# Kernel optimization log

Hardware: AMD Instinct MI355X
Metric: run time of the kernel (lower is better)

## Reference

```python
import jax, jax.numpy as jnp
import numpy as np

N_NODES = 50000
N_EDGES = 600000
IN_DIM = 128
OUT_DIM = 128
NEG_SLOPE = 0.2
LN_EPS = 1e-5


def setup_inputs() -> dict:
    key = jax.random.key(0)
    ks = jax.random.split(key, 8)
    x = jax.random.normal(ks[0], (N_NODES, IN_DIM), dtype=jnp.float32)
    edge_index = jax.random.randint(ks[1], (2, N_EDGES), 0, N_NODES, dtype=jnp.int64)
    glorot = float(np.sqrt(6.0 / (IN_DIM + OUT_DIM)))
    W_l = jax.random.uniform(ks[2], (IN_DIM, OUT_DIM), jnp.float32, -glorot, glorot)
    W_r = jax.random.uniform(ks[3], (IN_DIM, OUT_DIM), jnp.float32, -glorot, glorot)
    att = jax.random.uniform(ks[4], (OUT_DIM,), jnp.float32, -glorot, glorot)
    bias = jnp.zeros((OUT_DIM,), jnp.float32)
    ln_gamma = jnp.ones((OUT_DIM,), jnp.float32)
    ln_beta = jnp.zeros((OUT_DIM,), jnp.float32)
    return {"x": x, "edge_index": edge_index, "W_l": W_l, "W_r": W_r,
            "att": att, "bias": bias, "ln_gamma": ln_gamma, "ln_beta": ln_beta}


def _gatv2_ln(x, edge_index, W_l, W_r, att, bias, ln_gamma, ln_beta):
    N = x.shape[0]
    # add self loops (PyG GATv2Conv default add_self_loops=True)
    loop = jnp.arange(N, dtype=edge_index.dtype)
    src = jnp.concatenate([edge_index[0], loop])  # [E+N]
    dst = jnp.concatenate([edge_index[1], loop])
    x_l = x @ W_l  # [N, D] transformed source features
    x_r = x @ W_r  # [N, D] transformed target features
    # GATv2 edge score: e_ij = a^T LeakyReLU(x_l[src] + x_r[dst])
    h = jax.nn.leaky_relu(x_l[src] + x_r[dst], NEG_SLOPE)  # [E+N, D]
    e = h @ att  # [E+N]
    # segment softmax over incoming edges of each dst node
    m = jax.lax.stop_gradient(jax.ops.segment_max(e, dst, num_segments=N))
    ex = jnp.exp(e - m[dst])
    denom = jax.ops.segment_sum(ex, dst, num_segments=N)
    alpha = ex / denom[dst]  # [E+N] (denom > 0 thanks to self loops)
    # weighted scatter-add aggregation (dropout=0.1 is inference no-op)
    out = jax.ops.segment_sum(alpha[:, None] * x_l[src], dst, num_segments=N)
    out = out + bias  # heads=1, concat=False -> mean over 1 head = identity
    # LayerNorm over feature dim
    mu = jnp.mean(out, axis=-1, keepdims=True)
    var = jnp.var(out, axis=-1, keepdims=True)
    return (out - mu) * jax.lax.rsqrt(var + LN_EPS) * ln_gamma + ln_beta


def reference(x, edge_index, W_l, W_r, att, bias, ln_gamma, ln_beta):
    return _gatv2_ln(x, edge_index, W_l, W_r, att, bias, ln_gamma, ln_beta)
```

## Files before the change

### kernel.cpp

```cpp
#include <hip/hip_runtime.h>
#include <hip/hip_bf16.h>


constexpr int NN  = 50000;
constexpr int NE  = 600000;
constexpr int D   = 128;
constexpr int CAP = 64;
constexpr int MT  = 80;
constexpr int GEMM_THREADS = 320;

typedef __attribute__((ext_vector_type(8))) short bf16x8;
typedef __attribute__((ext_vector_type(4))) float f32x4;

__device__ __forceinline__ ushort f2bf(float f) {
  uint u = __builtin_bit_cast(uint, f);
  return (ushort)((u + 0x7FFFu + ((u >> 16) & 1u)) >> 16);
}
__device__ __forceinline__ float2 bf2f2(uint u) {
  float2 r;
  r.x = __builtin_bit_cast(float, u << 16);
  r.y = __builtin_bit_cast(float, u & 0xFFFF0000u);
  return r;
}

__global__ __launch_bounds__(256) void k_wpack(const float* __restrict__ Wl,
    const float* __restrict__ Wr, ushort* __restrict__ wpk) {
  const int t = blockIdx.x * 256 + threadIdx.x;
  if (t >= 2 * 4 * 8 * 64) return;
  const int lane = t & 63;
  const int ct   = (t >> 6) & 7;
  const int ks   = (t >> 9) & 3;
  const int wh   = t >> 11;
  const float* W = wh ? Wr : Wl;
  const int c  = ct * 16 + (lane & 15);
  const int k0 = ks * 32 + (lane >> 4) * 8;
  ushort v[8];
#pragma unroll
  for (int j = 0; j < 8; ++j) v[j] = f2bf(W[(k0 + j) * D + c]);
  *(bf16x8*)&wpk[(size_t)t * 8] = *(bf16x8*)v;
}

__global__ __launch_bounds__(GEMM_THREADS) void k_gemm(const float* __restrict__ x,
    const ushort* __restrict__ wpk, ushort* __restrict__ xl,
    float* __restrict__ xr) {
  __shared__ __align__(16) ushort axs[MT * D];
  const int t = threadIdx.x;
  const int row0 = blockIdx.x * MT;
  for (int ch = t; ch < MT * 16; ch += GEMM_THREADS) {
    const int r = ch >> 4, kc = ch & 15;
    const float4* src = (const float4*)&x[(size_t)(row0 + r) * D + kc * 8];
    const float4 f0 = src[0], f1 = src[1];
    ushort pk[8];
    pk[0] = f2bf(f0.x); pk[1] = f2bf(f0.y); pk[2] = f2bf(f0.z); pk[3] = f2bf(f0.w);
    pk[4] = f2bf(f1.x); pk[5] = f2bf(f1.y); pk[6] = f2bf(f1.z); pk[7] = f2bf(f1.w);
    uint byte = (uint)(r * 256 + kc * 16);
    byte ^= (uint)((r & 7) << 4);
    *(bf16x8*)((char*)axs + byte) = *(bf16x8*)pk;
  }
  __syncthreads();
  const int w = t >> 6, l = t & 63;
  f32x4 accl[8], accr[8];
#pragma unroll
  for (int ct = 0; ct < 8; ++ct) { accl[ct] = (f32x4)0.f; accr[ct] = (f32x4)0.f; }
  const bf16x8* wv = (const bf16x8*)wpk;
  const int rloc = w * 16 + (l & 15);
#pragma unroll
  for (int ks = 0; ks < 4; ++ks) {
    uint byte = (uint)(rloc * 256 + ks * 64 + ((l >> 4) << 4));
    byte ^= (uint)((rloc & 7) << 4);
    const bf16x8 a = *(const bf16x8*)((const char*)axs + byte);
#pragma unroll
    for (int ct = 0; ct < 8; ++ct) {
      const bf16x8 bl = wv[((0 * 4 + ks) * 8 + ct) * 64 + l];
      const bf16x8 br = wv[((1 * 4 + ks) * 8 + ct) * 64 + l];
      accl[ct] = __builtin_amdgcn_mfma_f32_16x16x32_bf16(a, bl, accl[ct], 0, 0, 0);
      accr[ct] = __builtin_amdgcn_mfma_f32_16x16x32_bf16(a, br, accr[ct], 0, 0, 0);
    }
  }
  const int rl0 = w * 16 + ((l >> 4) << 2);
  const int cl  = l & 15;
#pragma unroll
  for (int ct = 0; ct < 8; ++ct) {
    const int col = ct * 16 + cl;
#pragma unroll
    for (int i = 0; i < 4; ++i) {
      const size_t o = (size_t)(row0 + rl0 + i) * D + col;
      xl[o] = f2bf(accl[ct][i]);
      xr[o] = accr[ct][i];
    }
  }
}

__global__ __launch_bounds__(256) void k_init(int* __restrict__ cnt,
                                              int* __restrict__ eidx) {
  const int n = blockIdx.x * 256 + threadIdx.x;
  if (n < NN) { cnt[n] = 1; eidx[n * CAP] = n; }
}

__global__ __launch_bounds__(256) void k_fill(const int* __restrict__ ei,
    int* __restrict__ cnt, int* __restrict__ eidx) {
  const int e = blockIdx.x * 256 + threadIdx.x;
  if (e < NE) {
    const int src = ei[e];
    const int dst = ei[NE + e];
    const int pos = atomicAdd(&cnt[dst], 1);
    if (pos < CAP) eidx[dst * CAP + pos] = src;
  }
}

__global__ __launch_bounds__(256) void k_node(const int* __restrict__ cnt,
    const int* __restrict__ eidx,
    const ushort* __restrict__ xl, const float* __restrict__ xr,
    const float* __restrict__ att, const float* __restrict__ bias,
    const float* __restrict__ gamma, const float* __restrict__ beta,
    float* __restrict__ out) {
  const int n = blockIdx.x * 4 + (threadIdx.x >> 6);
  const int lane = threadIdx.x & 63;
  const float2 vr = *(const float2*)&xr[(size_t)n * D + lane * 2];
  const float2 av = *(const float2*)&att[lane * 2];
  const int m    = min(cnt[n], CAP);
  const int base = n * CAP;
  constexpr float LOG2E = 1.4426950408889634f;
  float accx = 0.f, accy = 0.f, den = 0.f;
  int p = 0;
  for (; p + 4 <= m; p += 4) {
    const int4 s4 = *(const int4*)&eidx[base + p];
    const float2 v0 = bf2f2(*(const uint*)&xl[(size_t)s4.x * D + lane * 2]);
    const float2 v1 = bf2f2(*(const uint*)&xl[(size_t)s4.y * D + lane * 2]);
    const float2 v2 = bf2f2(*(const uint*)&xl[(size_t)s4.z * D + lane * 2]);
    const float2 v3 = bf2f2(*(const uint*)&xl[(size_t)s4.w * D + lane * 2]);
    float a0 = v0.x + vr.x, b0 = v0.y + vr.y;
    float a1 = v1.x + vr.x, b1 = v1.y + vr.y;
    float a2 = v2.x + vr.x, b2 = v2.y + vr.y;
    float a3 = v3.x + vr.x, b3 = v3.y + vr.y;
    a0 = (a0 > 0.f) ? a0 : 0.2f * a0;  b0 = (b0 > 0.f) ? b0 : 0.2f * b0;
    a1 = (a1 > 0.f) ? a1 : 0.2f * a1;  b1 = (b1 > 0.f) ? b1 : 0.2f * b1;
    a2 = (a2 > 0.f) ? a2 : 0.2f * a2;  b2 = (b2 > 0.f) ? b2 : 0.2f * b2;
    a3 = (a3 > 0.f) ? a3 : 0.2f * a3;  b3 = (b3 > 0.f) ? b3 : 0.2f * b3;
    float s0 = fmaf(a0, av.x, b0 * av.y);
    float s1 = fmaf(a1, av.x, b1 * av.y);
    float s2 = fmaf(a2, av.x, b2 * av.y);
    float s3 = fmaf(a3, av.x, b3 * av.y);
#pragma unroll
    for (int off = 32; off > 0; off >>= 1) {
      s0 += __shfl_xor(s0, off);
      s1 += __shfl_xor(s1, off);
      s2 += __shfl_xor(s2, off);
      s3 += __shfl_xor(s3, off);
    }
    const float e0 = exp2f(s0 * LOG2E);
    const float e1 = exp2f(s1 * LOG2E);
    const float e2 = exp2f(s2 * LOG2E);
    const float e3 = exp2f(s3 * LOG2E);
    den += (e0 + e1) + (e2 + e3);
    accx = fmaf(e0, v0.x, fmaf(e1, v1.x, fmaf(e2, v2.x, fmaf(e3, v3.x, accx))));
    accy = fmaf(e0, v0.y, fmaf(e1, v1.y, fmaf(e2, v2.y, fmaf(e3, v3.y, accy))));
  }
  for (; p < m; ++p) {
    const int src = eidx[base + p];
    const float2 v = bf2f2(*(const uint*)&xl[(size_t)src * D + lane * 2]);
    float a = v.x + vr.x, b = v.y + vr.y;
    a = (a > 0.f) ? a : 0.2f * a;
    b = (b > 0.f) ? b : 0.2f * b;
    float s = fmaf(a, av.x, b * av.y);
#pragma unroll
    for (int off = 32; off > 0; off >>= 1) s += __shfl_xor(s, off);
    const float e = exp2f(s * LOG2E);
    den += e;
    accx = fmaf(e, v.x, accx);
    accy = fmaf(e, v.y, accy);
  }
  const float inv = 1.0f / den;
  const float2 bv = *(const float2*)&bias[lane * 2];
  const float vx = fmaf(accx, inv, bv.x);
  const float vy = fmaf(accy, inv, bv.y);
  float s  = vx + vy;
  float sq = vx * vx + vy * vy;
#pragma unroll
  for (int off = 32; off > 0; off >>= 1) {
    s  += __shfl_xor(s, off);
    sq += __shfl_xor(sq, off);
  }
  const float mean = s * (1.0f / D);
  const float var  = sq * (1.0f / D) - mean * mean;
  const float rstd = rsqrtf(var + 1e-5f);
  const float2 g  = *(const float2*)&gamma[lane * 2];
  const float2 be = *(const float2*)&beta[lane * 2];
  float2 o;
  o.x = (vx - mean) * rstd * g.x + be.x;
  o.y = (vy - mean) * rstd * g.y + be.y;
  *(float2*)&out[(size_t)n * D + lane * 2] = o;
}

extern "C" void kernel_launch(void* const* d_in, const int* in_sizes, int n_in,
                              void* d_out, int out_size, void* d_ws, size_t ws_size,
                              hipStream_t stream) {
  const float* x     = (const float*)d_in[0];
  const int*   ei    = (const int*)d_in[1];
  const float* Wl    = (const float*)d_in[2];
  const float* Wr    = (const float*)d_in[3];
  const float* att   = (const float*)d_in[4];
  const float* bias  = (const float*)d_in[5];
  const float* gamma = (const float*)d_in[6];
  const float* beta  = (const float*)d_in[7];
  float* out = (float*)d_out;

  char* ws = (char*)d_ws;
  float*  xr   = (float*)ws;
  ushort* xl   = (ushort*)(xr + (size_t)NN * D);
  int*    eidx = (int*)(xl + (size_t)NN * D);
  int*    cnt  = eidx + (size_t)NN * CAP;
  ushort* wpk  = (ushort*)(cnt + NN);

  k_wpack<<<16, 256, 0, stream>>>(Wl, Wr, wpk);
  k_init<<<(NN + 255) / 256, 256, 0, stream>>>(cnt, eidx);
  k_gemm<<<NN / MT, GEMM_THREADS, 0, stream>>>(x, wpk, xl, xr);
  k_fill<<<(NE + 255) / 256, 256, 0, stream>>>(ei, cnt, eidx);
  k_node<<<NN / 4, 256, 0, stream>>>(cnt, eidx, xl, xr, att, bias, gamma,
                                     beta, out);
}
```

Baseline: 197.1 us.

## Fuse GEMM with edge fill and process eight edges per wave in node kernel

Merges the GEMM and the edge-bucketing fill into one launch: extra blocks handle the edges, and self loops are now inserted through atomics after a memset instead of by a separate init kernel. The node kernel is reorganised so each wave handles 8 edges at once, with each 8-lane group loading 16 features as 32-byte vector loads. This cuts the per-edge cross-lane reductions and adds memory-level parallelism. The cost is more registers and a reduction across lane groups at the end, and the self loop can now land in any slot, so summation order becomes nondeterministic.

After: 215.5 us. 1.09x slower.

```diff
diff --git a/kernel.cpp b/kernel.cpp
--- a/kernel.cpp
+++ b/kernel.cpp
@@ -5,9 +5,12 @@
 constexpr int NN  = 50000;
 constexpr int NE  = 600000;
 constexpr int D   = 128;
+constexpr int NT  = NE + NN;
 constexpr int CAP = 64;
 constexpr int MT  = 80;
 constexpr int GEMM_THREADS = 320;
+constexpr int GEMM_BLOCKS  = NN / MT;
+constexpr int FILL_BLOCKS  = (NT + GEMM_THREADS - 1) / GEMM_THREADS;
 
 typedef __attribute__((ext_vector_type(8))) short bf16x8;
 typedef __attribute__((ext_vector_type(4))) float f32x4;
@@ -16,12 +19,8 @@
   uint u = __builtin_bit_cast(uint, f);
   return (ushort)((u + 0x7FFFu + ((u >> 16) & 1u)) >> 16);
 }
-__device__ __forceinline__ float2 bf2f2(uint u) {
-  float2 r;
-  r.x = __builtin_bit_cast(float, u << 16);
-  r.y = __builtin_bit_cast(float, u & 0xFFFF0000u);
-  return r;
-}
+__device__ __forceinline__ float bflo(uint u) { return __builtin_bit_cast(float, u << 16); }
+__device__ __forceinline__ float bfhi(uint u) { return __builtin_bit_cast(float, u & 0xFFFF0000u); }
 
 __global__ __launch_bounds__(256) void k_wpack(const float* __restrict__ Wl,
     const float* __restrict__ Wr, ushort* __restrict__ wpk) {
@@ -40,9 +39,21 @@
   *(bf16x8*)&wpk[(size_t)t * 8] = *(bf16x8*)v;
 }
 
-__global__ __launch_bounds__(GEMM_THREADS) void k_gemm(const float* __restrict__ x,
+__global__ __launch_bounds__(GEMM_THREADS) void k_mega(const float* __restrict__ x,
     const ushort* __restrict__ wpk, ushort* __restrict__ xl,
-    float* __restrict__ xr) {
+    float* __restrict__ xr, const int* __restrict__ ei,
+    int* __restrict__ cnt, int* __restrict__ eidx) {
+  if (blockIdx.x >= GEMM_BLOCKS) {
+    const int e = (blockIdx.x - GEMM_BLOCKS) * GEMM_THREADS + threadIdx.x;
+    if (e < NT) {
+      int src, dst;
+      if (e < NE) { src = ei[e]; dst = ei[NE + e]; }
+      else        { src = e - NE; dst = src; }
+      const int pos = atomicAdd(&cnt[dst], 1);
+      if (pos < CAP) eidx[dst * CAP + pos] = src;
+    }
+    return;
+  }
   __shared__ __align__(16) ushort axs[MT * D];
   const int t = threadIdx.x;
   const int row0 = blockIdx.x * MT;
@@ -91,23 +102,6 @@
   }
 }
 
-__global__ __launch_bounds__(256) void k_init(int* __restrict__ cnt,
-                                              int* __restrict__ eidx) {
-  const int n = blockIdx.x * 256 + threadIdx.x;
-  if (n < NN) { cnt[n] = 1; eidx[n * CAP] = n; }
-}
-
-__global__ __launch_bounds__(256) void k_fill(const int* __restrict__ ei,
-    int* __restrict__ cnt, int* __restrict__ eidx) {
-  const int e = blockIdx.x * 256 + threadIdx.x;
-  if (e < NE) {
-    const int src = ei[e];
-    const int dst = ei[NE + e];
-    const int pos = atomicAdd(&cnt[dst], 1);
-    if (pos < CAP) eidx[dst * CAP + pos] = src;
-  }
-}
-
 __global__ __launch_bounds__(256) void k_node(const int* __restrict__ cnt,
     const int* __restrict__ eidx,
     const ushort* __restrict__ xl, const float* __restrict__ xr,
@@ -116,80 +110,92 @@
     float* __restrict__ out) {
   const int n = blockIdx.x * 4 + (threadIdx.x >> 6);
   const int lane = threadIdx.x & 63;
-  const float2 vr = *(const float2*)&xr[(size_t)n * D + lane * 2];
-  const float2 av = *(const float2*)&att[lane * 2];
+  const int eg = lane & 7;
+  const int ls = lane >> 3;
+  const int d0 = ls * 16;
+  constexpr float LOG2E = 1.4426950408889634f;
+
+  float vr[16], av[16];
+#pragma unroll
+  for (int j = 0; j < 16; j += 4) {
+    *(float4*)&vr[j] = *(const float4*)&xr[(size_t)n * D + d0 + j];
+    *(float4*)&av[j] = *(const float4*)&att[d0 + j];
+  }
   const int m    = min(cnt[n], CAP);
   const int base = n * CAP;
-  constexpr float LOG2E = 1.4426950408889634f;
-  float accx = 0.f, accy = 0.f, den = 0.f;
-  int p = 0;
-  for (; p + 4 <= m; p += 4) {
-    const int4 s4 = *(const int4*)&eidx[base + p];
-    const float2 v0 = bf2f2(*(const uint*)&xl[(size_t)s4.x * D + lane * 2]);
-    const float2 v1 = bf2f2(*(const uint*)&xl[(size_t)s4.y * D + lane * 2]);
-    const float2 v2 = bf2f2(*(const uint*)&xl[(size_t)s4.z * D + lane * 2]);
-    const float2 v3 = bf2f2(*(const uint*)&xl[(size_t)s4.w * D + lane * 2]);
-    float a0 = v0.x + vr.x, b0 = v0.y + vr.y;
-    float a1 = v1.x + vr.x, b1 = v1.y + vr.y;
-    float a2 = v2.x + vr.x, b2 = v2.y + vr.y;
-    float a3 = v3.x + vr.x, b3 = v3.y + vr.y;
-    a0 = (a0 > 0.f) ? a0 : 0.2f * a0;  b0 = (b0 > 0.f) ? b0 : 0.2f * b0;
-    a1 = (a1 > 0.f) ? a1 : 0.2f * a1;  b1 = (b1 > 0.f) ? b1 : 0.2f * b1;
-    a2 = (a2 > 0.f) ? a2 : 0.2f * a2;  b2 = (b2 > 0.f) ? b2 : 0.2f * b2;
-    a3 = (a3 > 0.f) ? a3 : 0.2f * a3;  b3 = (b3 > 0.f) ? b3 : 0.2f * b3;
-    float s0 = fmaf(a0, av.x, b0 * av.y);
-    float s1 = fmaf(a1, av.x, b1 * av.y);
-    float s2 = fmaf(a2, av.x, b2 * av.y);
-    float s3 = fmaf(a3, av.x, b3 * av.y);
-#pragma unroll
-    for (int off = 32; off > 0; off >>= 1) {
-      s0 += __shfl_xor(s0, off);
-      s1 += __shfl_xor(s1, off);
-      s2 += __shfl_xor(s2, off);
-      s3 += __shfl_xor(s3, off);
-    }
-    const float e0 = exp2f(s0 * LOG2E);
-    const float e1 = exp2f(s1 * LOG2E);
-    const float e2 = exp2f(s2 * LOG2E);
-    const float e3 = exp2f(s3 * LOG2E);
-    den += (e0 + e1) + (e2 + e3);
-    accx = fmaf(e0, v0.x, fmaf(e1, v1.x, fmaf(e2, v2.x, fmaf(e3, v3.x, accx))));
-    accy = fmaf(e0, v0.y, fmaf(e1, v1.y, fmaf(e2, v2.y, fmaf(e3, v3.y, accy))));
-  }
-  for (; p < m; ++p) {
-    const int src = eidx[base + p];
-    const float2 v = bf2f2(*(const uint*)&xl[(size_t)src * D + lane * 2]);
-    float a = v.x + vr.x, b = v.y + vr.y;
-    a = (a > 0.f) ? a : 0.2f * a;
-    b = (b > 0.f) ? b : 0.2f * b;
-    float s = fmaf(a, av.x, b * av.y);
-#pragma unroll
-    for (int off = 32; off > 0; off >>= 1) s += __shfl_xor(s, off);
-    const float e = exp2f(s * LOG2E);
+  float acc[16];
+#pragma unroll
+  for (int j = 0; j < 16; ++j) acc[j] = 0.f;
+  float den = 0.f;
+
+  for (int p0 = 0; p0 < m; p0 += 8) {
+    const int pe  = p0 + eg;
+    const bool act = (pe < m);
+    const int src = act ? eidx[base + pe] : 0;
+    const uint4 u0 = *(const uint4*)&xl[(size_t)src * D + d0];
+    const uint4 u1 = *(const uint4*)&xl[(size_t)src * D + d0 + 8];
+    float v[16];
+    v[0]=bflo(u0.x); v[1]=bfhi(u0.x); v[2]=bflo(u0.y); v[3]=bfhi(u0.y);
+    v[4]=bflo(u0.z); v[5]=bfhi(u0.z); v[6]=bflo(u0.w); v[7]=bfhi(u0.w);
+    v[8]=bflo(u1.x); v[9]=bfhi(u1.x); v[10]=bflo(u1.y); v[11]=bfhi(u1.y);
+    v[12]=bflo(u1.z); v[13]=bfhi(u1.z); v[14]=bflo(u1.w); v[15]=bfhi(u1.w);
+    float s = 0.f;
+#pragma unroll
+    for (int j = 0; j < 16; ++j) {
+      float h = v[j] + vr[j];
+      h = fmaxf(h, 0.2f * h);
+      s = fmaf(h, av[j], s);
+    }
+    s += __shfl_xor(s, 8);
+    s += __shfl_xor(s, 16);
+    s += __shfl_xor(s, 32);
+    const float e = act ? exp2f(s * LOG2E) : 0.f;
     den += e;
-    accx = fmaf(e, v.x, accx);
-    accy = fmaf(e, v.y, accy);
-  }
+#pragma unroll
+    for (int j = 0; j < 16; ++j) acc[j] = fmaf(e, v[j], acc[j]);
+  }
+#pragma unroll
+  for (int j = 0; j < 16; ++j) {
+    acc[j] += __shfl_xor(acc[j], 1);
+    acc[j] += __shfl_xor(acc[j], 2);
+    acc[j] += __shfl_xor(acc[j], 4);
+  }
+  den += __shfl_xor(den, 1);
+  den += __shfl_xor(den, 2);
+  den += __shfl_xor(den, 4);
   const float inv = 1.0f / den;
-  const float2 bv = *(const float2*)&bias[lane * 2];
-  const float vx = fmaf(accx, inv, bv.x);
-  const float vy = fmaf(accy, inv, bv.y);
-  float s  = vx + vy;
-  float sq = vx * vx + vy * vy;
-#pragma unroll
-  for (int off = 32; off > 0; off >>= 1) {
-    s  += __shfl_xor(s, off);
-    sq += __shfl_xor(sq, off);
-  }
-  const float mean = s * (1.0f / D);
+
+  float o[16];
+#pragma unroll
+  for (int j = 0; j < 16; j += 4) {
+    const float4 bv = *(const float4*)&bias[d0 + j];
+    o[j]   = fmaf(acc[j],   inv, bv.x);
+    o[j+1] = fmaf(acc[j+1], inv, bv.y);
+    o[j+2] = fmaf(acc[j+2], inv, bv.z);
+    o[j+3] = fmaf(acc[j+3], inv, bv.w);
+  }
+  float sm = 0.f, sq = 0.f;
+#pragma unroll
+  for (int j = 0; j < 16; ++j) { sm += o[j]; sq = fmaf(o[j], o[j], sq); }
+  sm += __shfl_xor(sm, 8);  sq += __shfl_xor(sq, 8);
+  sm += __shfl_xor(sm, 16); sq += __shfl_xor(sq, 16);
+  sm += __shfl_xor(sm, 32); sq += __shfl_xor(sq, 32);
+  const float mean = sm * (1.0f / D);
   const float var  = sq * (1.0f / D) - mean * mean;
   const float rstd = rsqrtf(var + 1e-5f);
-  const float2 g  = *(const float2*)&gamma[lane * 2];
-  const float2 be = *(const float2*)&beta[lane * 2];
-  float2 o;
-  o.x = (vx - mean) * rstd * g.x + be.x;
-  o.y = (vy - mean) * rstd * g.y + be.y;
-  *(float2*)&out[(size_t)n * D + lane * 2] = o;
+  if (eg == 0) {
+#pragma unroll
+    for (int j = 0; j < 16; j += 4) {
+      const float4 g  = *(const float4*)&gamma[d0 + j];
+      const float4 be = *(const float4*)&beta[d0 + j];
+      float4 ov;
+      ov.x = (o[j]   - mean) * rstd * g.x + be.x;
+      ov.y = (o[j+1] - mean) * rstd * g.y + be.y;
+      ov.z = (o[j+2] - mean) * rstd * g.z + be.z;
+      ov.w = (o[j+3] - mean) * rstd * g.w + be.w;
+      *(float4*)&out[(size_t)n * D + d0 + j] = ov;
+    }
+  }
 }
 
 extern "C" void kernel_launch(void* const* d_in, const int* in_sizes, int n_in,
@@ -212,10 +218,10 @@
   int*    cnt  = eidx + (size_t)NN * CAP;
   ushort* wpk  = (ushort*)(cnt + NN);
 
+  hipMemsetAsync(cnt, 0, NN * sizeof(int), stream);
   k_wpack<<<16, 256, 0, stream>>>(Wl, Wr, wpk);
-  k_init<<<(NN + 255) / 256, 256, 0, stream>>>(cnt, eidx);
-  k_gemm<<<NN / MT, GEMM_THREADS, 0, stream>>>(x, wpk, xl, xr);
-  k_fill<<<(NE + 255) / 256, 256, 0, stream>>>(ei, cnt, eidx);
+  k_mega<<<GEMM_BLOCKS + FILL_BLOCKS, GEMM_THREADS, 0, stream>>>(
+      x, wpk, xl, xr, ei, cnt, eidx);
   k_node<<<NN / 4, 256, 0, stream>>>(cnt, eidx, xl, xr, att, bias, gamma,
                                      beta, out);
 }
```
